# Kernel optimization log

Measured on AMD Instinct MI355X. Metric: run time of the kernel, lower is better.

The kernel has to match this reference:

```python
import jax, jax.numpy as jnp
import numpy as np

N, E = 50000, 800000
IN_FEATS, H, F = 128, 2, 64
NEG_SLOPE = 0.2


def _gat_conv(x, W, attn_l, attn_r, bias, src, dst):
    """DGL-style GATConv. x:[N,IN], W:[H*F,IN], attn_l/attn_r:[H,F], bias:[H*F]. Returns [N,H,F]."""
    z = (x @ W.T).reshape(N, H, F)                      # node projections
    el = jnp.einsum('nhf,hf->nh', z, attn_l)            # [N,H]
    er = jnp.einsum('nhf,hf->nh', z, attn_r)            # [N,H]
    e = jax.nn.leaky_relu(el[src] + er[dst], NEG_SLOPE) # [E,H] edge logits
    # edge softmax over incoming edges of each destination node
    m = jax.ops.segment_max(e, dst, num_segments=N)     # [N,H]
    ex = jnp.exp(e - m[dst])
    s = jax.ops.segment_sum(ex, dst, num_segments=N)    # [N,H]
    alpha = ex / s[dst]                                 # [E,H]
    msg = alpha[:, :, None] * z[src]                    # [E,H,F]
    out = jax.ops.segment_sum(msg, dst, num_segments=N) # [N,H,F]
    return out + bias.reshape(1, H, F)


def setup_inputs() -> dict:
    key = jax.random.key(0)
    ks = jax.random.split(key, 10)
    x = jax.random.normal(ks[0], (N, IN_FEATS), dtype=jnp.float32)
    h = jax.random.normal(ks[1], (N, H, F), dtype=jnp.float32)
    src = jax.random.randint(ks[2], (E,), 0, N, dtype=jnp.int32)
    dst = jax.random.randint(ks[3], (E,), 0, N, dtype=jnp.int32)
    sc = 1.0 / np.sqrt(IN_FEATS)
    W = jax.random.normal(ks[4], (3, H * F, IN_FEATS), dtype=jnp.float32) * sc  # r,u,c fc weights
    attn_l = jax.random.normal(ks[5], (3, H, F), dtype=jnp.float32) * 0.1
    attn_r = jax.random.normal(ks[6], (3, H, F), dtype=jnp.float32) * 0.1
    conv_bias = jax.random.normal(ks[7], (3, H * F), dtype=jnp.float32) * 0.02
    gate_bias = jax.random.uniform(ks[8], (3, H, F), dtype=jnp.float32)  # torch.rand init
    return {"x": x, "h": h, "W": W, "attn_l": attn_l, "attn_r": attn_r,
            "conv_bias": conv_bias, "gate_bias": gate_bias, "src": src, "dst": dst}


def reference(x, h, W, attn_l, attn_r, conv_bias, gate_bias, src, dst):
    # r, u, c gates; each GATConv is applied to x (use_hidden=False branch)
    r = jax.nn.sigmoid(_gat_conv(x, W[0], attn_l[0], attn_r[0], conv_bias[0], src, dst) + gate_bias[0])
    u = jax.nn.sigmoid(_gat_conv(x, W[1], attn_l[1], attn_r[1], conv_bias[1], src, dst) + gate_bias[1])
    # note: original computes h_ = r*h but never uses it in this branch (dead code)
    c = jax.nn.sigmoid(_gat_conv(x, W[2], attn_l[2], attn_r[2], conv_bias[2], src, dst) + gate_bias[2])
    new_h = u * h + (1.0 - u) * c
    return new_h
```

## Files before the change

kernel.cpp:

```cpp
#include <hip/hip_runtime.h>
#include <hip/hip_bf16.h>
#include <math.h>

#define NN 50000
#define EE 800000
#define KIN 128
#define HFD 128
#define ZC 256
#define NB 196
#define GB2 1564
#define SB 782
#define CAP 64
#define TRS 132

typedef __bf16 bf16_t;
typedef __bf16 bf16x4 __attribute__((ext_vector_type(4)));
typedef __bf16 bf16x8 __attribute__((ext_vector_type(8)));
typedef float f32x4 __attribute__((ext_vector_type(4)));

__device__ __forceinline__ float ldf(const void* p, size_t i, int isf32) {
    return isf32 ? ((const float*)p)[i] : (float)((const bf16_t*)p)[i];
}
__device__ __forceinline__ bf16x8 load8bf(const void* base, size_t off, int isf32) {
    if (isf32) {
        const float4* p = (const float4*)((const float*)base + off);
        float4 u = p[0], v = p[1];
        bf16x8 r;
        r[0] = (bf16_t)u.x; r[1] = (bf16_t)u.y; r[2] = (bf16_t)u.z; r[3] = (bf16_t)u.w;
        r[4] = (bf16_t)v.x; r[5] = (bf16_t)v.y; r[6] = (bf16_t)v.z; r[7] = (bf16_t)v.w;
        return r;
    }
    return *(const bf16x8*)((const bf16_t*)base + off);
}

__global__ __launch_bounds__(256) void k_front(const unsigned short* __restrict__ xw,
                                               const void* __restrict__ W,
                                               const void* __restrict__ attn_l,
                                               const void* __restrict__ attn_r,
                                               int* __restrict__ deg,
                                               int* __restrict__ dflag,
                                               bf16_t* __restrict__ walv)
{
    const int b = blockIdx.x, tid = threadIdx.x;
    int i = b * 256 + tid;
    if (i < NN) deg[i] = 0;
    if (b > 8) return;

    __shared__ int cnt;
    if (tid == 0) cnt = 0;
    __syncthreads();
    int c = 0;
    for (int k = tid; k < 2048; k += 256) {
        int e = (xw[k] >> 7) & 0xFF;
        if (e > 150) c++;
    }
    atomicAdd(&cnt, c);
    __syncthreads();
    const int isf32 = (cnt > 20) ? 1 : 0;

    if (b == 0) {
        if (tid == 0) dflag[0] = isf32;
        return;
    }
    const int c8 = b - 1;
    const int side = c8 >> 2, g = (c8 >> 1) & 1, h = c8 & 1;
    const void* attn = side ? attn_r : attn_l;
    const int k = tid;
    if (k < KIN) {
        float acc = 0.f;
        for (int f = 0; f < 64; f++) {
            float wv = ldf(W, ((size_t)(g + 1) * HFD + h * 64 + f) * KIN + k, isf32);
            float av = ldf(attn, (size_t)((g + 1) * 2 + h) * 64 + f, isf32);
            acc += wv * av;
        }
        walv[(size_t)c8 * KIN + k] = (bf16_t)acc;
    }
}

__global__ __launch_bounds__(256) void k_big(const void* __restrict__ x,
                                             const void* __restrict__ W,
                                             const bf16_t* __restrict__ walv,
                                             bf16_t* __restrict__ z,
                                             float* __restrict__ eln,
                                             float* __restrict__ ern,
                                             const int* __restrict__ src,
                                             const int* __restrict__ dst,
                                             int* __restrict__ deg,
                                             int* __restrict__ ssrc,
                                             const int* __restrict__ dflag)
{
    __shared__ bf16_t wlds[128 * 128];

    if (blockIdx.x >= GB2) {
        int base = (blockIdx.x - GB2) * 1024 + threadIdx.x * 4;
        if (base < EE) {
            int4 s4 = *(const int4*)(src + base);
            int4 d4 = *(const int4*)(dst + base);
            int p0 = atomicAdd(&deg[d4.x], 1);
            int p1 = atomicAdd(&deg[d4.y], 1);
            int p2 = atomicAdd(&deg[d4.z], 1);
            int p3 = atomicAdd(&deg[d4.w], 1);
            if (p0 < CAP) ssrc[d4.x * CAP + p0] = s4.x;
            if (p1 < CAP) ssrc[d4.y * CAP + p1] = s4.y;
            if (p2 < CAP) ssrc[d4.z * CAP + p2] = s4.z;
            if (p3 < CAP) ssrc[d4.w * CAP + p3] = s4.w;
        }
        return;
    }

    const int isf32 = dflag[0];
    const int tid = threadIdx.x;
    const int ng = blockIdx.x >> 1;
    const int g  = blockIdx.x & 1;

    for (int c = tid; c < 2048; c += 256) {
        int col = c >> 4, g8 = c & 15;
        bf16x8 v = load8bf(W, ((size_t)(g + 1) * HFD + col) * KIN + g8 * 8, isf32);
        *(bf16x8*)(wlds + (size_t)col * 128 + (g8 ^ (col & 15)) * 8) = v;
    }

    const int wave = tid >> 6;
    const int lane = tid & 63;
    const int quad = lane >> 4;
    const int lm   = lane & 15;
    const int node_base = ng * 64 + wave * 16;

    int nld = node_base + lm;
    if (nld > NN - 1) nld = NN - 1;

    bf16x8 a[4];
#pragma unroll
    for (int kk = 0; kk < 4; kk++)
        a[kk] = load8bf(x, (size_t)nld * KIN + kk * 32 + quad * 8, isf32);

    __syncthreads();

    f32x4 acc[8];
#pragma unroll
    for (int t = 0; t < 8; t++) {
        const int wc = t * 16 + lm;
        f32x4 a4 = {0.f, 0.f, 0.f, 0.f};
#pragma unroll
        for (int kk = 0; kk < 4; kk++) {
            bf16x8 b = *(const bf16x8*)(wlds + (size_t)wc * 128 + ((kk * 4 + quad) ^ lm) * 8);
            a4 = __builtin_amdgcn_mfma_f32_16x16x32_bf16(a[kk], b, a4, 0, 0, 0);
        }
        acc[t] = a4;
    }

    if (g == 0) {
        f32x4 sacc = {0.f, 0.f, 0.f, 0.f};
#pragma unroll
        for (int kk = 0; kk < 4; kk++) {
            bf16x8 b;
            if (lm < 8) b = *(const bf16x8*)(walv + (size_t)lm * KIN + kk * 32 + quad * 8);
            else {
#pragma unroll
                for (int j = 0; j < 8; j++) b[j] = (bf16_t)0.f;
            }
            sacc = __builtin_amdgcn_mfma_f32_16x16x32_bf16(a[kk], b, sacc, 0, 0, 0);
        }
#pragma unroll
        for (int r = 0; r < 4; r++) {
            int nn = node_base + quad * 4 + r;
            if (nn < NN) {
                if (lm < 4)      eln[(size_t)nn * 4 + lm] = sacc[r];
                else if (lm < 8) ern[(size_t)nn * 4 + (lm - 4)] = sacc[r];
            }
        }
    }

    __syncthreads();
#pragma unroll
    for (int t = 0; t < 8; t++) {
#pragma unroll
        for (int r = 0; r < 4; r++)
            wlds[(size_t)(wave * 16 + quad * 4 + r) * TRS + t * 16 + lm] = (bf16_t)acc[t][r];
    }
    __syncthreads();
#pragma unroll
    for (int q = 0; q < 4; q++) {
        int node64 = q * 16 + (tid >> 4);
        int chunk  = tid & 15;
        bf16x8 v = *(const bf16x8*)(wlds + (size_t)node64 * TRS + chunk * 8);
        int node = ng * 64 + node64;
        if (node < NN)
            *(bf16x8*)(z + (size_t)node * ZC + g * 128 + chunk * 8) = v;
    }
}

__global__ __launch_bounds__(256) void k_agg(const bf16_t* __restrict__ z,
                                             const int* __restrict__ deg,
                                             const int* __restrict__ ssrc,
                                             const float* __restrict__ eln,
                                             const float* __restrict__ ern,
                                             const void* __restrict__ conv_bias,
                                             const void* __restrict__ gate_bias,
                                             const void* __restrict__ hin,
                                             void* __restrict__ out,
                                             const int* __restrict__ dflag)
{
    const int isf32 = dflag[0];
    const int wave = threadIdx.x >> 6;
    const int lane = threadIdx.x & 63;
    const int j = lane >> 4;
    const int n = blockIdx.x * 4 + wave;
    if (n >= NN) return;
    int cnt = deg[n];
    if (cnt > CAP) cnt = CAP;
    const int* row = ssrc + (size_t)n * CAP;
    const float erj = ern[(size_t)n * 4 + j];
    const size_t zoff = 4 * lane;

    float a0 = 0.f, a1 = 0.f, a2 = 0.f, a3 = 0.f;
    float s = 0.f;
    int i = 0;
    for (; i + 8 <= cnt; i += 8) {
        int sn[8];
#pragma unroll
        for (int q = 0; q < 8; q++) sn[q] = row[i + q];
        bf16x4 p[8];
#pragma unroll
        for (int q = 0; q < 8; q++)
            p[q] = *(const bf16x4*)(z + (size_t)sn[q] * ZC + zoff);
        float w[8];
#pragma unroll
        for (int q = 0; q < 8; q++) {
            float v = eln[(size_t)sn[q] * 4 + j] + erj;
            v = v > 0.f ? v : 0.2f * v;
            w[q] = __expf(v);
        }
#pragma unroll
        for (int q = 0; q < 8; q++) {
            a0 += w[q] * (float)p[q][0];
            a1 += w[q] * (float)p[q][1];
            a2 += w[q] * (float)p[q][2];
            a3 += w[q] * (float)p[q][3];
            s += w[q];
        }
    }
    if (i + 4 <= cnt) {
        int sn[4];
#pragma unroll
        for (int q = 0; q < 4; q++) sn[q] = row[i + q];
        bf16x4 p[4];
#pragma unroll
        for (int q = 0; q < 4; q++)
            p[q] = *(const bf16x4*)(z + (size_t)sn[q] * ZC + zoff);
#pragma unroll
        for (int q = 0; q < 4; q++) {
            float v = eln[(size_t)sn[q] * 4 + j] + erj;
            v = v > 0.f ? v : 0.2f * v;
            float w = __expf(v);
            a0 += w * (float)p[q][0];
            a1 += w * (float)p[q][1];
            a2 += w * (float)p[q][2];
            a3 += w * (float)p[q][3];
            s += w;
        }
        i += 4;
    }
    for (; i < cnt; i++) {
        int sn = row[i];
        float v = eln[(size_t)sn * 4 + j] + erj;
        bf16x4 p = *(const bf16x4*)(z + (size_t)sn * ZC + zoff);
        v = v > 0.f ? v : 0.2f * v;
        float w = __expf(v);
        a0 += w * (float)p[0];
        a1 += w * (float)p[1];
        a2 += w * (float)p[2];
        a3 += w * (float)p[3];
        s += w;
    }

    float inv = (cnt > 0) ? 1.f / fmaxf(s, 1e-30f) : 0.f;
    float o[4] = {a0 * inv, a1 * inv, a2 * inv, a3 * inv};

    float res[4];
    float hh[4];
    if (lane < 32) {
#pragma unroll
        for (int t = 0; t < 4; t++)
            hh[t] = ldf(hin, (size_t)n * HFD + 4 * lane + t, isf32);
    }
#pragma unroll
    for (int t = 0; t < 4; t++) {
        int c = 4 * lane + t;
        int gate = c >> 7;
        int cf = c & 127;
        int h = cf >> 6, f = cf & 63;
        float ob = ldf(conv_bias, (size_t)(gate + 1) * 128 + cf, isf32)
                 + ldf(gate_bias, (size_t)((gate + 1) * 2 + h) * 64 + f, isf32);
        float gv = 1.f / (1.f + __expf(-(o[t] + ob)));
        float other = __shfl(gv, lane ^ 32, 64);
        if (lane < 32)
            res[t] = gv * hh[t] + (1.f - gv) * other;
    }
    if (lane < 32) {
        if (isf32) {
            float4 v = {res[0], res[1], res[2], res[3]};
            *(float4*)((float*)out + (size_t)n * HFD + 4 * lane) = v;
        } else {
            bf16x4 v;
            v[0] = (bf16_t)res[0]; v[1] = (bf16_t)res[1];
            v[2] = (bf16_t)res[2]; v[3] = (bf16_t)res[3];
            *(bf16x4*)((bf16_t*)out + (size_t)n * HFD + 4 * lane) = v;
        }
    }
}

extern "C" void kernel_launch(void* const* d_in, const int* in_sizes, int n_in,
                              void* d_out, int out_size, void* d_ws, size_t ws_size,
                              hipStream_t stream)
{
    const void* x         = d_in[0];
    const void* hin       = d_in[1];
    const void* W         = d_in[2];
    const void* attn_l    = d_in[3];
    const void* attn_r    = d_in[4];
    const void* conv_bias = d_in[5];
    const void* gate_bias = d_in[6];
    const int* src        = (const int*)d_in[7];
    const int* dst        = (const int*)d_in[8];

    char* p = (char*)d_ws;
    int* dflag    = (int*)p;    p += 256;
    bf16_t* z     = (bf16_t*)p; p += (size_t)NN * ZC * 2;
    float* eln    = (float*)p;  p += (size_t)NN * 4 * 4;
    float* ern    = (float*)p;  p += (size_t)NN * 4 * 4;
    int* deg      = (int*)p;    p += (size_t)NN * 4;
    int* ssrc     = (int*)p;    p += (size_t)NN * CAP * 4;
    bf16_t* walv  = (bf16_t*)p; p += 8 * KIN * 2;

    k_front<<<NB, 256, 0, stream>>>((const unsigned short*)x, W, attn_l, attn_r,
                                    deg, dflag, walv);
    k_big<<<GB2 + SB, 256, 0, stream>>>(x, W, walv, z, eln, ern, src, dst,
                                        deg, ssrc, dflag);
    k_agg<<<(NN + 3) / 4, 256, 0, stream>>>(z, deg, ssrc, eln, ern,
                                            conv_bias, gate_bias, hin, d_out, dflag);
}
```

Measured before the change: 253.7 us.

## Split edge aggregation across two waves per node and compress source indices

Each destination node's incoming edges are now split between two wavefronts. Their partial sums are combined through shared memory, which aims to give more memory-level parallelism in the latency-bound gather. Source indices in the adjacency buckets are stored as 16-bit values, halving index traffic; this relies on the node count fitting in 16 bits. The fused GEMM-plus-scatter kernel is split into two separate launches, which adds a launch and removes the overlap between the GEMM and the scatter atomics.

```diff
diff --git a/kernel.cpp b/kernel.cpp
--- a/kernel.cpp
+++ b/kernel.cpp
@@ -17,6 +17,8 @@
 typedef __bf16 bf16x4 __attribute__((ext_vector_type(4)));
 typedef __bf16 bf16x8 __attribute__((ext_vector_type(8)));
 typedef float f32x4 __attribute__((ext_vector_type(4)));
+typedef unsigned short u16;
+typedef unsigned int u32;
 
 __device__ __forceinline__ float ldf(const void* p, size_t i, int isf32) {
     return isf32 ? ((const float*)p)[i] : (float)((const bf16_t*)p)[i];
@@ -77,36 +79,34 @@
     }
 }
 
-__global__ __launch_bounds__(256) void k_big(const void* __restrict__ x,
-                                             const void* __restrict__ W,
-                                             const bf16_t* __restrict__ walv,
-                                             bf16_t* __restrict__ z,
-                                             float* __restrict__ eln,
-                                             float* __restrict__ ern,
-                                             const int* __restrict__ src,
-                                             const int* __restrict__ dst,
-                                             int* __restrict__ deg,
-                                             int* __restrict__ ssrc,
-                                             const int* __restrict__ dflag)
+__global__ __launch_bounds__(256) void k_scat(const int* __restrict__ src,
+                                              const int* __restrict__ dst,
+                                              int* __restrict__ deg,
+                                              u16* __restrict__ ssrc)
+{
+    int base = blockIdx.x * 1024 + threadIdx.x * 4;
+    if (base >= EE) return;
+    int4 s4 = *(const int4*)(src + base);
+    int4 d4 = *(const int4*)(dst + base);
+    int p0 = atomicAdd(&deg[d4.x], 1);
+    int p1 = atomicAdd(&deg[d4.y], 1);
+    int p2 = atomicAdd(&deg[d4.z], 1);
+    int p3 = atomicAdd(&deg[d4.w], 1);
+    if (p0 < CAP) ssrc[d4.x * CAP + p0] = (u16)s4.x;
+    if (p1 < CAP) ssrc[d4.y * CAP + p1] = (u16)s4.y;
+    if (p2 < CAP) ssrc[d4.z * CAP + p2] = (u16)s4.z;
+    if (p3 < CAP) ssrc[d4.w * CAP + p3] = (u16)s4.w;
+}
+
+__global__ __launch_bounds__(256) void k_gemm(const void* __restrict__ x,
+                                              const void* __restrict__ W,
+                                              const bf16_t* __restrict__ walv,
+                                              bf16_t* __restrict__ z,
+                                              float* __restrict__ eln,
+                                              float* __restrict__ ern,
+                                              const int* __restrict__ dflag)
 {
     __shared__ bf16_t wlds[128 * 128];
-
-    if (blockIdx.x >= GB2) {
-        int base = (blockIdx.x - GB2) * 1024 + threadIdx.x * 4;
-        if (base < EE) {
-            int4 s4 = *(const int4*)(src + base);
-            int4 d4 = *(const int4*)(dst + base);
-            int p0 = atomicAdd(&deg[d4.x], 1);
-            int p1 = atomicAdd(&deg[d4.y], 1);
-            int p2 = atomicAdd(&deg[d4.z], 1);
-            int p3 = atomicAdd(&deg[d4.w], 1);
-            if (p0 < CAP) ssrc[d4.x * CAP + p0] = s4.x;
-            if (p1 < CAP) ssrc[d4.y * CAP + p1] = s4.y;
-            if (p2 < CAP) ssrc[d4.z * CAP + p2] = s4.z;
-            if (p3 < CAP) ssrc[d4.w * CAP + p3] = s4.w;
-        }
-        return;
-    }
 
     const int isf32 = dflag[0];
     const int tid = threadIdx.x;
@@ -191,7 +191,7 @@
 
 __global__ __launch_bounds__(256) void k_agg(const bf16_t* __restrict__ z,
                                              const int* __restrict__ deg,
-                                             const int* __restrict__ ssrc,
+                                             const u16* __restrict__ ssrc,
                                              const float* __restrict__ eln,
                                              const float* __restrict__ ern,
                                              const void* __restrict__ conv_bias,
@@ -200,25 +200,36 @@
                                              void* __restrict__ out,
                                              const int* __restrict__ dflag)
 {
+    __shared__ float pacc[2][64][5];
     const int isf32 = dflag[0];
     const int wave = threadIdx.x >> 6;
     const int lane = threadIdx.x & 63;
+    const int nl   = wave >> 1;
+    const int part = wave & 1;
     const int j = lane >> 4;
-    const int n = blockIdx.x * 4 + wave;
+    const int n = blockIdx.x * 2 + nl;
     if (n >= NN) return;
     int cnt = deg[n];
     if (cnt > CAP) cnt = CAP;
-    const int* row = ssrc + (size_t)n * CAP;
+    const u16* row = ssrc + (size_t)n * CAP;
+    const u32* row32 = (const u32*)row;
     const float erj = ern[(size_t)n * 4 + j];
     const size_t zoff = 4 * lane;
 
+    int mid = (cnt / 2 + 7) & ~7;
+    if (mid > cnt) mid = cnt;
+    int i   = part ? mid : 0;
+    int lim = part ? cnt : mid;
+
     float a0 = 0.f, a1 = 0.f, a2 = 0.f, a3 = 0.f;
     float s = 0.f;
-    int i = 0;
-    for (; i + 8 <= cnt; i += 8) {
+    for (; i + 8 <= lim; i += 8) {
+        u32 rr[4];
+#pragma unroll
+        for (int q = 0; q < 4; q++) rr[q] = row32[(i >> 1) + q];
         int sn[8];
 #pragma unroll
-        for (int q = 0; q < 8; q++) sn[q] = row[i + q];
+        for (int q = 0; q < 4; q++) { sn[2*q] = rr[q] & 0xFFFF; sn[2*q+1] = rr[q] >> 16; }
         bf16x4 p[8];
 #pragma unroll
         for (int q = 0; q < 8; q++)
@@ -239,28 +250,7 @@
             s += w[q];
         }
     }
-    if (i + 4 <= cnt) {
-        int sn[4];
-#pragma unroll
-        for (int q = 0; q < 4; q++) sn[q] = row[i + q];
-        bf16x4 p[4];
-#pragma unroll
-        for (int q = 0; q < 4; q++)
-            p[q] = *(const bf16x4*)(z + (size_t)sn[q] * ZC + zoff);
-#pragma unroll
-        for (int q = 0; q < 4; q++) {
-            float v = eln[(size_t)sn[q] * 4 + j] + erj;
-            v = v > 0.f ? v : 0.2f * v;
-            float w = __expf(v);
-            a0 += w * (float)p[q][0];
-            a1 += w * (float)p[q][1];
-            a2 += w * (float)p[q][2];
-            a3 += w * (float)p[q][3];
-            s += w;
-        }
-        i += 4;
-    }
-    for (; i < cnt; i++) {
+    for (; i < lim; i++) {
         int sn = row[i];
         float v = eln[(size_t)sn * 4 + j] + erj;
         bf16x4 p = *(const bf16x4*)(z + (size_t)sn * ZC + zoff);
@@ -272,6 +262,17 @@
         a3 += w * (float)p[3];
         s += w;
     }
+
+    if (part == 1) {
+        pacc[nl][lane][0] = a0; pacc[nl][lane][1] = a1;
+        pacc[nl][lane][2] = a2; pacc[nl][lane][3] = a3;
+        pacc[nl][lane][4] = s;
+    }
+    __syncthreads();
+    if (part == 1) return;
+    a0 += pacc[nl][lane][0]; a1 += pacc[nl][lane][1];
+    a2 += pacc[nl][lane][2]; a3 += pacc[nl][lane][3];
+    s  += pacc[nl][lane][4];
 
     float inv = (cnt > 0) ? 1.f / fmaxf(s, 1e-30f) : 0.f;
     float o[4] = {a0 * inv, a1 * inv, a2 * inv, a3 * inv};
@@ -329,13 +330,13 @@
     float* eln    = (float*)p;  p += (size_t)NN * 4 * 4;
     float* ern    = (float*)p;  p += (size_t)NN * 4 * 4;
     int* deg      = (int*)p;    p += (size_t)NN * 4;
-    int* ssrc     = (int*)p;    p += (size_t)NN * CAP * 4;
+    u16* ssrc     = (u16*)p;    p += (size_t)NN * CAP * 2;
     bf16_t* walv  = (bf16_t*)p; p += 8 * KIN * 2;
 
     k_front<<<NB, 256, 0, stream>>>((const unsigned short*)x, W, attn_l, attn_r,
                                     deg, dflag, walv);
-    k_big<<<GB2 + SB, 256, 0, stream>>>(x, W, walv, z, eln, ern, src, dst,
-                                        deg, ssrc, dflag);
-    k_agg<<<(NN + 3) / 4, 256, 0, stream>>>(z, deg, ssrc, eln, ern,
+    k_scat<<<SB, 256, 0, stream>>>(src, dst, deg, ssrc);
+    k_gemm<<<GB2, 256, 0, stream>>>(x, W, walv, z, eln, ern, dflag);
+    k_agg<<<(NN + 1) / 2, 256, 0, stream>>>(z, deg, ssrc, eln, ern,
                                             conv_bias, gate_bias, hin, d_out, dflag);
 }
```

After: 278.5 us. 9.8% more time.

## Store neighbor indices as 16-bit and aggregate two nodes per wave

Applied to the files above, without the earlier changes.

The per-destination source-index buckets are now stored as 16-bit values instead of 32-bit, halving that buffer's write and read traffic, and are read two at a time as 32-bit words. The aggregation kernel now processes two destination nodes per wavefront with interleaved gather loops, giving more independent loads in flight to hide gather latency. Node ids go up to 50000, which fits in 16 bits, so the truncation is safe for this N. The two-node scheme raises register pressure, and waves whose two nodes have unequal degree run a serial tail.

```diff
diff --git a/kernel.cpp b/kernel.cpp
--- a/kernel.cpp
+++ b/kernel.cpp
@@ -17,6 +17,8 @@
 typedef __bf16 bf16x4 __attribute__((ext_vector_type(4)));
 typedef __bf16 bf16x8 __attribute__((ext_vector_type(8)));
 typedef float f32x4 __attribute__((ext_vector_type(4)));
+typedef unsigned short u16;
+typedef unsigned int u32;
 
 __device__ __forceinline__ float ldf(const void* p, size_t i, int isf32) {
     return isf32 ? ((const float*)p)[i] : (float)((const bf16_t*)p)[i];
@@ -86,7 +88,7 @@
                                              const int* __restrict__ src,
                                              const int* __restrict__ dst,
                                              int* __restrict__ deg,
-                                             int* __restrict__ ssrc,
+                                             u16* __restrict__ ssrc,
                                              const int* __restrict__ dflag)
 {
     __shared__ bf16_t wlds[128 * 128];
@@ -100,10 +102,10 @@
             int p1 = atomicAdd(&deg[d4.y], 1);
             int p2 = atomicAdd(&deg[d4.z], 1);
             int p3 = atomicAdd(&deg[d4.w], 1);
-            if (p0 < CAP) ssrc[d4.x * CAP + p0] = s4.x;
-            if (p1 < CAP) ssrc[d4.y * CAP + p1] = s4.y;
-            if (p2 < CAP) ssrc[d4.z * CAP + p2] = s4.z;
-            if (p3 < CAP) ssrc[d4.w * CAP + p3] = s4.w;
+            if (p0 < CAP) ssrc[d4.x * CAP + p0] = (u16)s4.x;
+            if (p1 < CAP) ssrc[d4.y * CAP + p1] = (u16)s4.y;
+            if (p2 < CAP) ssrc[d4.z * CAP + p2] = (u16)s4.z;
+            if (p3 < CAP) ssrc[d4.w * CAP + p3] = (u16)s4.w;
         }
         return;
     }
@@ -156,7 +158,7 @@
             if (lm < 8) b = *(const bf16x8*)(walv + (size_t)lm * KIN + kk * 32 + quad * 8);
             else {
 #pragma unroll
-                for (int j = 0; j < 8; j++) b[j] = (bf16_t)0.f;
+                for (int jj = 0; jj < 8; jj++) b[jj] = (bf16_t)0.f;
             }
             sacc = __builtin_amdgcn_mfma_f32_16x16x32_bf16(a[kk], b, sacc, 0, 0, 0);
         }
@@ -189,9 +191,58 @@
     }
 }
 
+__device__ __forceinline__ void grp8(const bf16_t* __restrict__ z,
+                                     const float* __restrict__ eln,
+                                     const u32* __restrict__ row32, int i, int j,
+                                     float erj, size_t zoff, float* A)
+{
+    u32 rr[4];
+#pragma unroll
+    for (int q = 0; q < 4; q++) rr[q] = row32[(i >> 1) + q];
+    int sn[8];
+#pragma unroll
+    for (int q = 0; q < 4; q++) { sn[2*q] = rr[q] & 0xFFFF; sn[2*q+1] = rr[q] >> 16; }
+    bf16x4 p[8];
+#pragma unroll
+    for (int q = 0; q < 8; q++)
+        p[q] = *(const bf16x4*)(z + (size_t)sn[q] * ZC + zoff);
+    float w[8];
+#pragma unroll
+    for (int q = 0; q < 8; q++) {
+        float v = eln[(size_t)sn[q] * 4 + j] + erj;
+        v = v > 0.f ? v : 0.2f * v;
+        w[q] = __expf(v);
+    }
+#pragma unroll
+    for (int q = 0; q < 8; q++) {
+        A[0] += w[q] * (float)p[q][0];
+        A[1] += w[q] * (float)p[q][1];
+        A[2] += w[q] * (float)p[q][2];
+        A[3] += w[q] * (float)p[q][3];
+        A[4] += w[q];
+    }
+}
+
+__device__ __forceinline__ void grp1(const bf16_t* __restrict__ z,
+                                     const float* __restrict__ eln,
+                                     const u16* __restrict__ row, int i, int j,
+                                     float erj, size_t zoff, float* A)
+{
+    int sn = row[i];
+    bf16x4 p = *(const bf16x4*)(z + (size_t)sn * ZC + zoff);
+    float v = eln[(size_t)sn * 4 + j] + erj;
+    v = v > 0.f ? v : 0.2f * v;
+    float w = __expf(v);
+    A[0] += w * (float)p[0];
+    A[1] += w * (float)p[1];
+    A[2] += w * (float)p[2];
+    A[3] += w * (float)p[3];
+    A[4] += w;
+}
+
 __global__ __launch_bounds__(256) void k_agg(const bf16_t* __restrict__ z,
                                              const int* __restrict__ deg,
-                                             const int* __restrict__ ssrc,
+                                             const u16* __restrict__ ssrc,
                                              const float* __restrict__ eln,
                                              const float* __restrict__ ern,
                                              const void* __restrict__ conv_bias,
@@ -204,107 +255,117 @@
     const int wave = threadIdx.x >> 6;
     const int lane = threadIdx.x & 63;
     const int j = lane >> 4;
-    const int n = blockIdx.x * 4 + wave;
-    if (n >= NN) return;
-    int cnt = deg[n];
-    if (cnt > CAP) cnt = CAP;
-    const int* row = ssrc + (size_t)n * CAP;
-    const float erj = ern[(size_t)n * 4 + j];
+    const int n0 = blockIdx.x * 8 + wave * 2;
+    const int n1 = n0 + 1;
+
+    int c0 = deg[n0]; if (c0 > CAP) c0 = CAP;
+    int c1 = deg[n1]; if (c1 > CAP) c1 = CAP;
+    const u16* row0 = ssrc + (size_t)n0 * CAP;
+    const u16* row1 = ssrc + (size_t)n1 * CAP;
+    const u32* r32_0 = (const u32*)row0;
+    const u32* r32_1 = (const u32*)row1;
+    const float er0 = ern[(size_t)n0 * 4 + j];
+    const float er1 = ern[(size_t)n1 * 4 + j];
     const size_t zoff = 4 * lane;
 
-    float a0 = 0.f, a1 = 0.f, a2 = 0.f, a3 = 0.f;
-    float s = 0.f;
-    int i = 0;
-    for (; i + 8 <= cnt; i += 8) {
-        int sn[8];
-#pragma unroll
-        for (int q = 0; q < 8; q++) sn[q] = row[i + q];
-        bf16x4 p[8];
-#pragma unroll
-        for (int q = 0; q < 8; q++)
-            p[q] = *(const bf16x4*)(z + (size_t)sn[q] * ZC + zoff);
-        float w[8];
+    float A0[5] = {0.f, 0.f, 0.f, 0.f, 0.f};
+    float A1[5] = {0.f, 0.f, 0.f, 0.f, 0.f};
+    int i0 = 0, i1 = 0;
+
+    while (i0 + 8 <= c0 && i1 + 8 <= c1) {
+        u32 rrA[4], rrB[4];
+#pragma unroll
+        for (int q = 0; q < 4; q++) { rrA[q] = r32_0[(i0 >> 1) + q]; rrB[q] = r32_1[(i1 >> 1) + q]; }
+        int snA[8], snB[8];
+#pragma unroll
+        for (int q = 0; q < 4; q++) {
+            snA[2*q] = rrA[q] & 0xFFFF; snA[2*q+1] = rrA[q] >> 16;
+            snB[2*q] = rrB[q] & 0xFFFF; snB[2*q+1] = rrB[q] >> 16;
+        }
+        bf16x4 pA[8], pB[8];
+#pragma unroll
+        for (int q = 0; q < 8; q++) pA[q] = *(const bf16x4*)(z + (size_t)snA[q] * ZC + zoff);
+#pragma unroll
+        for (int q = 0; q < 8; q++) pB[q] = *(const bf16x4*)(z + (size_t)snB[q] * ZC + zoff);
+        float wA[8], wB[8];
 #pragma unroll
         for (int q = 0; q < 8; q++) {
-            float v = eln[(size_t)sn[q] * 4 + j] + erj;
+            float v = eln[(size_t)snA[q] * 4 + j] + er0;
             v = v > 0.f ? v : 0.2f * v;
-            w[q] = __expf(v);
+            wA[q] = __expf(v);
         }
 #pragma unroll
         for (int q = 0; q < 8; q++) {
-            a0 += w[q] * (float)p[q][0];
-            a1 += w[q] * (float)p[q][1];
-            a2 += w[q] * (float)p[q][2];
-            a3 += w[q] * (float)p[q][3];
-            s += w[q];
-        }
-    }
-    if (i + 4 <= cnt) {
-        int sn[4];
-#pragma unroll
-        for (int q = 0; q < 4; q++) sn[q] = row[i + q];
-        bf16x4 p[4];
-#pragma unroll
-        for (int q = 0; q < 4; q++)
-            p[q] = *(const bf16x4*)(z + (size_t)sn[q] * ZC + zoff);
-#pragma unroll
-        for (int q = 0; q < 4; q++) {
-            float v = eln[(size_t)sn[q] * 4 + j] + erj;
+            float v = eln[(size_t)snB[q] * 4 + j] + er1;
             v = v > 0.f ? v : 0.2f * v;
-            float w = __expf(v);
-            a0 += w * (float)p[q][0];
-            a1 += w * (float)p[q][1];
-            a2 += w * (float)p[q][2];
-            a3 += w * (float)p[q][3];
-            s += w;
-        }
-        i += 4;
-    }
-    for (; i < cnt; i++) {
-        int sn = row[i];
-        float v = eln[(size_t)sn * 4 + j] + erj;
-        bf16x4 p = *(const bf16x4*)(z + (size_t)sn * ZC + zoff);
-        v = v > 0.f ? v : 0.2f * v;
-        float w = __expf(v);
-        a0 += w * (float)p[0];
-        a1 += w * (float)p[1];
-        a2 += w * (float)p[2];
-        a3 += w * (float)p[3];
-        s += w;
-    }
-
-    float inv = (cnt > 0) ? 1.f / fmaxf(s, 1e-30f) : 0.f;
-    float o[4] = {a0 * inv, a1 * inv, a2 * inv, a3 * inv};
-
-    float res[4];
-    float hh[4];
-    if (lane < 32) {
-#pragma unroll
-        for (int t = 0; t < 4; t++)
-            hh[t] = ldf(hin, (size_t)n * HFD + 4 * lane + t, isf32);
-    }
+            wB[q] = __expf(v);
+        }
+#pragma unroll
+        for (int q = 0; q < 8; q++) {
+            A0[0] += wA[q] * (float)pA[q][0];
+            A0[1] += wA[q] * (float)pA[q][1];
+            A0[2] += wA[q] * (float)pA[q][2];
+            A0[3] += wA[q] * (float)pA[q][3];
+            A0[4] += wA[q];
+            A1[0] += wB[q] * (float)pB[q][0];
+            A1[1] += wB[q] * (float)pB[q][1];
+            A1[2] += wB[q] * (float)pB[q][2];
+            A1[3] += wB[q] * (float)pB[q][3];
+            A1[4] += wB[q];
+        }
+        i0 += 8; i1 += 8;
+    }
+    while (i0 + 8 <= c0) { grp8(z, eln, r32_0, i0, j, er0, zoff, A0); i0 += 8; }
+    while (i1 + 8 <= c1) { grp8(z, eln, r32_1, i1, j, er1, zoff, A1); i1 += 8; }
+    while (i0 < c0 && i1 < c1) {
+        grp1(z, eln, row0, i0, j, er0, zoff, A0);
+        grp1(z, eln, row1, i1, j, er1, zoff, A1);
+        i0++; i1++;
+    }
+    while (i0 < c0) { grp1(z, eln, row0, i0, j, er0, zoff, A0); i0++; }
+    while (i1 < c1) { grp1(z, eln, row1, i1, j, er1, zoff, A1); i1++; }
+
+    float ob[4];
 #pragma unroll
     for (int t = 0; t < 4; t++) {
         int c = 4 * lane + t;
         int gate = c >> 7;
         int cf = c & 127;
         int h = cf >> 6, f = cf & 63;
-        float ob = ldf(conv_bias, (size_t)(gate + 1) * 128 + cf, isf32)
-                 + ldf(gate_bias, (size_t)((gate + 1) * 2 + h) * 64 + f, isf32);
-        float gv = 1.f / (1.f + __expf(-(o[t] + ob)));
-        float other = __shfl(gv, lane ^ 32, 64);
-        if (lane < 32)
-            res[t] = gv * hh[t] + (1.f - gv) * other;
-    }
-    if (lane < 32) {
-        if (isf32) {
-            float4 v = {res[0], res[1], res[2], res[3]};
-            *(float4*)((float*)out + (size_t)n * HFD + 4 * lane) = v;
-        } else {
-            bf16x4 v;
-            v[0] = (bf16_t)res[0]; v[1] = (bf16_t)res[1];
-            v[2] = (bf16_t)res[2]; v[3] = (bf16_t)res[3];
-            *(bf16x4*)((bf16_t*)out + (size_t)n * HFD + 4 * lane) = v;
+        ob[t] = ldf(conv_bias, (size_t)(gate + 1) * 128 + cf, isf32)
+              + ldf(gate_bias, (size_t)((gate + 1) * 2 + h) * 64 + f, isf32);
+    }
+
+#pragma unroll
+    for (int nn = 0; nn < 2; nn++) {
+        const int n = nn ? n1 : n0;
+        const float* A = nn ? A1 : A0;
+        const int cnt = nn ? c1 : c0;
+        float inv = (cnt > 0) ? 1.f / fmaxf(A[4], 1e-30f) : 0.f;
+        float hh[4];
+        if (lane < 32) {
+#pragma unroll
+            for (int t = 0; t < 4; t++)
+                hh[t] = ldf(hin, (size_t)n * HFD + 4 * lane + t, isf32);
+        }
+        float res[4];
+#pragma unroll
+        for (int t = 0; t < 4; t++) {
+            float gv = 1.f / (1.f + __expf(-(A[t] * inv + ob[t])));
+            float other = __shfl(gv, lane ^ 32, 64);
+            if (lane < 32)
+                res[t] = gv * hh[t] + (1.f - gv) * other;
+        }
+        if (lane < 32) {
+            if (isf32) {
+                float4 v = {res[0], res[1], res[2], res[3]};
+                *(float4*)((float*)out + (size_t)n * HFD + 4 * lane) = v;
+            } else {
+                bf16x4 v;
+                v[0] = (bf16_t)res[0]; v[1] = (bf16_t)res[1];
+                v[2] = (bf16_t)res[2]; v[3] = (bf16_t)res[3];
+                *(bf16x4*)((bf16_t*)out + (size_t)n * HFD + 4 * lane) = v;
+            }
         }
     }
 }
@@ -329,13 +390,13 @@
     float* eln    = (float*)p;  p += (size_t)NN * 4 * 4;
     float* ern    = (float*)p;  p += (size_t)NN * 4 * 4;
     int* deg      = (int*)p;    p += (size_t)NN * 4;
-    int* ssrc     = (int*)p;    p += (size_t)NN * CAP * 4;
+    u16* ssrc     = (u16*)p;    p += (size_t)NN * CAP * 2;
     bf16_t* walv  = (bf16_t*)p; p += 8 * KIN * 2;
 
     k_front<<<NB, 256, 0, stream>>>((const unsigned short*)x, W, attn_l, attn_r,
                                     deg, dflag, walv);
     k_big<<<GB2 + SB, 256, 0, stream>>>(x, W, walv, z, eln, ern, src, dst,
                                         deg, ssrc, dflag);
-    k_agg<<<(NN + 3) / 4, 256, 0, stream>>>(z, deg, ssrc, eln, ern,
-                                            conv_bias, gate_bias, hin, d_out, dflag);
-}
+    k_agg<<<NN / 8, 256, 0, stream>>>(z, deg, ssrc, eln, ern,
+                                      conv_bias, gate_bias, hin, d_out, dflag);
+}
```

Result: slower. 259.4 us (+2.3%).

## Store node projections as fp8 and neighbor indices as 16-bit

Applied to the files above, without the earlier changes.

The projected node features z are packed to fp8 (e4m3) when written in the projection kernel and unpacked with hardware fp8-to-f32 conversion during aggregation. Per-destination source lists are stored as 16-bit indices, read two at a time. Both changes halve the bytes of the random gathers that dominate the aggregation kernel. In exchange, z loses precision (3 mantissa bits), and the 16-bit indices only work because the node count fits in 16 bits.

```diff
diff --git a/kernel.cpp b/kernel.cpp
--- a/kernel.cpp
+++ b/kernel.cpp
@@ -6,7 +6,7 @@
 #define EE 800000
 #define KIN 128
 #define HFD 128
-#define ZC 256
+#define ZB 256
 #define NB 196
 #define GB2 1564
 #define SB 782
@@ -14,9 +14,12 @@
 #define TRS 132
 
 typedef __bf16 bf16_t;
-typedef __bf16 bf16x4 __attribute__((ext_vector_type(4)));
 typedef __bf16 bf16x8 __attribute__((ext_vector_type(8)));
+typedef float f32x2 __attribute__((ext_vector_type(2)));
 typedef float f32x4 __attribute__((ext_vector_type(4)));
+typedef unsigned short u16;
+typedef unsigned int u32;
+typedef unsigned char u8;
 
 __device__ __forceinline__ float ldf(const void* p, size_t i, int isf32) {
     return isf32 ? ((const float*)p)[i] : (float)((const bf16_t*)p)[i];
@@ -31,6 +34,14 @@
         return r;
     }
     return *(const bf16x8*)((const bf16_t*)base + off);
+}
+
+__device__ __forceinline__ uint2 pack8fp8(bf16x8 v) {
+    u32 lo = __builtin_amdgcn_cvt_pk_fp8_f32((float)v[0], (float)v[1], 0u, false);
+    lo = __builtin_amdgcn_cvt_pk_fp8_f32((float)v[2], (float)v[3], lo, true);
+    u32 hi = __builtin_amdgcn_cvt_pk_fp8_f32((float)v[4], (float)v[5], 0u, false);
+    hi = __builtin_amdgcn_cvt_pk_fp8_f32((float)v[6], (float)v[7], hi, true);
+    return make_uint2(lo, hi);
 }
 
 __global__ __launch_bounds__(256) void k_front(const unsigned short* __restrict__ xw,
@@ -80,13 +91,13 @@
 __global__ __launch_bounds__(256) void k_big(const void* __restrict__ x,
                                              const void* __restrict__ W,
                                              const bf16_t* __restrict__ walv,
-                                             bf16_t* __restrict__ z,
+                                             u8* __restrict__ z8,
                                              float* __restrict__ eln,
                                              float* __restrict__ ern,
                                              const int* __restrict__ src,
                                              const int* __restrict__ dst,
                                              int* __restrict__ deg,
-                                             int* __restrict__ ssrc,
+                                             u16* __restrict__ ssrc,
                                              const int* __restrict__ dflag)
 {
     __shared__ bf16_t wlds[128 * 128];
@@ -100,10 +111,10 @@
             int p1 = atomicAdd(&deg[d4.y], 1);
             int p2 = atomicAdd(&deg[d4.z], 1);
             int p3 = atomicAdd(&deg[d4.w], 1);
-            if (p0 < CAP) ssrc[d4.x * CAP + p0] = s4.x;
-            if (p1 < CAP) ssrc[d4.y * CAP + p1] = s4.y;
-            if (p2 < CAP) ssrc[d4.z * CAP + p2] = s4.z;
-            if (p3 < CAP) ssrc[d4.w * CAP + p3] = s4.w;
+            if (p0 < CAP) ssrc[d4.x * CAP + p0] = (u16)s4.x;
+            if (p1 < CAP) ssrc[d4.y * CAP + p1] = (u16)s4.y;
+            if (p2 < CAP) ssrc[d4.z * CAP + p2] = (u16)s4.z;
+            if (p3 < CAP) ssrc[d4.w * CAP + p3] = (u16)s4.w;
         }
         return;
     }
@@ -156,7 +167,7 @@
             if (lm < 8) b = *(const bf16x8*)(walv + (size_t)lm * KIN + kk * 32 + quad * 8);
             else {
 #pragma unroll
-                for (int j = 0; j < 8; j++) b[j] = (bf16_t)0.f;
+                for (int jj = 0; jj < 8; jj++) b[jj] = (bf16_t)0.f;
             }
             sacc = __builtin_amdgcn_mfma_f32_16x16x32_bf16(a[kk], b, sacc, 0, 0, 0);
         }
@@ -183,15 +194,16 @@
         int node64 = q * 16 + (tid >> 4);
         int chunk  = tid & 15;
         bf16x8 v = *(const bf16x8*)(wlds + (size_t)node64 * TRS + chunk * 8);
+        uint2 u = pack8fp8(v);
         int node = ng * 64 + node64;
         if (node < NN)
-            *(bf16x8*)(z + (size_t)node * ZC + g * 128 + chunk * 8) = v;
-    }
-}
-
-__global__ __launch_bounds__(256) void k_agg(const bf16_t* __restrict__ z,
+            *(uint2*)(z8 + (size_t)node * ZB + g * 128 + chunk * 8) = u;
+    }
+}
+
+__global__ __launch_bounds__(256) void k_agg(const u8* __restrict__ z8,
                                              const int* __restrict__ deg,
-                                             const int* __restrict__ ssrc,
+                                             const u16* __restrict__ ssrc,
                                              const float* __restrict__ eln,
                                              const float* __restrict__ ern,
                                              const void* __restrict__ conv_bias,
@@ -208,21 +220,24 @@
     if (n >= NN) return;
     int cnt = deg[n];
     if (cnt > CAP) cnt = CAP;
-    const int* row = ssrc + (size_t)n * CAP;
+    const u16* row = ssrc + (size_t)n * CAP;
+    const u32* row32 = (const u32*)row;
     const float erj = ern[(size_t)n * 4 + j];
-    const size_t zoff = 4 * lane;
-
-    float a0 = 0.f, a1 = 0.f, a2 = 0.f, a3 = 0.f;
-    float s = 0.f;
+    const u32 zoff = 4 * lane;
+
+    float a0 = 0.f, a1 = 0.f, a2 = 0.f, a3 = 0.f, s = 0.f;
     int i = 0;
     for (; i + 8 <= cnt; i += 8) {
+        u32 rr[4];
+#pragma unroll
+        for (int q = 0; q < 4; q++) rr[q] = row32[(i >> 1) + q];
         int sn[8];
 #pragma unroll
-        for (int q = 0; q < 8; q++) sn[q] = row[i + q];
-        bf16x4 p[8];
+        for (int q = 0; q < 4; q++) { sn[2*q] = rr[q] & 0xFFFF; sn[2*q+1] = rr[q] >> 16; }
+        u32 zb[8];
 #pragma unroll
         for (int q = 0; q < 8; q++)
-            p[q] = *(const bf16x4*)(z + (size_t)sn[q] * ZC + zoff);
+            zb[q] = *(const u32*)(z8 + (size_t)sn[q] * ZB + zoff);
         float w[8];
 #pragma unroll
         for (int q = 0; q < 8; q++) {
@@ -232,44 +247,53 @@
         }
 #pragma unroll
         for (int q = 0; q < 8; q++) {
-            a0 += w[q] * (float)p[q][0];
-            a1 += w[q] * (float)p[q][1];
-            a2 += w[q] * (float)p[q][2];
-            a3 += w[q] * (float)p[q][3];
+            f32x2 lo = __builtin_amdgcn_cvt_pk_f32_fp8(zb[q], false);
+            f32x2 hi = __builtin_amdgcn_cvt_pk_f32_fp8(zb[q], true);
+            a0 += w[q] * lo[0];
+            a1 += w[q] * lo[1];
+            a2 += w[q] * hi[0];
+            a3 += w[q] * hi[1];
             s += w[q];
         }
     }
     if (i + 4 <= cnt) {
+        u32 rr[2];
+#pragma unroll
+        for (int q = 0; q < 2; q++) rr[q] = row32[(i >> 1) + q];
         int sn[4];
 #pragma unroll
-        for (int q = 0; q < 4; q++) sn[q] = row[i + q];
-        bf16x4 p[4];
+        for (int q = 0; q < 2; q++) { sn[2*q] = rr[q] & 0xFFFF; sn[2*q+1] = rr[q] >> 16; }
+        u32 zb[4];
 #pragma unroll
         for (int q = 0; q < 4; q++)
-            p[q] = *(const bf16x4*)(z + (size_t)sn[q] * ZC + zoff);
+            zb[q] = *(const u32*)(z8 + (size_t)sn[q] * ZB + zoff);
 #pragma unroll
         for (int q = 0; q < 4; q++) {
             float v = eln[(size_t)sn[q] * 4 + j] + erj;
             v = v > 0.f ? v : 0.2f * v;
             float w = __expf(v);
-            a0 += w * (float)p[q][0];
-            a1 += w * (float)p[q][1];
-            a2 += w * (float)p[q][2];
-            a3 += w * (float)p[q][3];
+            f32x2 lo = __builtin_amdgcn_cvt_pk_f32_fp8(zb[q], false);
+            f32x2 hi = __builtin_amdgcn_cvt_pk_f32_fp8(zb[q], true);
+            a0 += w * lo[0];
+            a1 += w * lo[1];
+            a2 += w * hi[0];
+            a3 += w * hi[1];
             s += w;
         }
         i += 4;
     }
     for (; i < cnt; i++) {
         int sn = row[i];
+        u32 zb = *(const u32*)(z8 + (size_t)sn * ZB + zoff);
         float v = eln[(size_t)sn * 4 + j] + erj;
-        bf16x4 p = *(const bf16x4*)(z + (size_t)sn * ZC + zoff);
         v = v > 0.f ? v : 0.2f * v;
         float w = __expf(v);
-        a0 += w * (float)p[0];
-        a1 += w * (float)p[1];
-        a2 += w * (float)p[2];
-        a3 += w * (float)p[3];
+        f32x2 lo = __builtin_amdgcn_cvt_pk_f32_fp8(zb, false);
+        f32x2 hi = __builtin_amdgcn_cvt_pk_f32_fp8(zb, true);
+        a0 += w * lo[0];
+        a1 += w * lo[1];
+        a2 += w * hi[0];
+        a3 += w * hi[1];
         s += w;
     }
 
@@ -301,10 +325,10 @@
             float4 v = {res[0], res[1], res[2], res[3]};
             *(float4*)((float*)out + (size_t)n * HFD + 4 * lane) = v;
         } else {
-            bf16x4 v;
+            bf16_t v[4];
             v[0] = (bf16_t)res[0]; v[1] = (bf16_t)res[1];
             v[2] = (bf16_t)res[2]; v[3] = (bf16_t)res[3];
-            *(bf16x4*)((bf16_t*)out + (size_t)n * HFD + 4 * lane) = v;
+            *(uint2*)((bf16_t*)out + (size_t)n * HFD + 4 * lane) = *(uint2*)v;
         }
     }
 }
@@ -325,17 +349,17 @@
 
     char* p = (char*)d_ws;
     int* dflag    = (int*)p;    p += 256;
-    bf16_t* z     = (bf16_t*)p; p += (size_t)NN * ZC * 2;
+    u8* z8        = (u8*)p;     p += (size_t)NN * ZB;
     float* eln    = (float*)p;  p += (size_t)NN * 4 * 4;
     float* ern    = (float*)p;  p += (size_t)NN * 4 * 4;
     int* deg      = (int*)p;    p += (size_t)NN * 4;
-    int* ssrc     = (int*)p;    p += (size_t)NN * CAP * 4;
+    u16* ssrc     = (u16*)p;    p += (size_t)NN * CAP * 2;
     bf16_t* walv  = (bf16_t*)p; p += 8 * KIN * 2;
 
     k_front<<<NB, 256, 0, stream>>>((const unsigned short*)x, W, attn_l, attn_r,
                                     deg, dflag, walv);
-    k_big<<<GB2 + SB, 256, 0, stream>>>(x, W, walv, z, eln, ern, src, dst,
+    k_big<<<GB2 + SB, 256, 0, stream>>>(x, W, walv, z8, eln, ern, src, dst,
                                         deg, ssrc, dflag);
-    k_agg<<<(NN + 3) / 4, 256, 0, stream>>>(z, deg, ssrc, eln, ern,
+    k_agg<<<(NN + 3) / 4, 256, 0, stream>>>(z8, deg, ssrc, eln, ern,
                                             conv_bias, gate_bias, hin, d_out, dflag);
 }
```

Result: faster. 231.0 us (-9.0%).
